# Performance work log

Hardware: AMD Instinct MI355X
Metric: run time of the kernel (lower is better)

The kernel has to match this reference:

```python
import jax, jax.numpy as jnp
import numpy as np

# Static configuration (mirrors the list of reconstruction_blocks)
B, F, D, H = 16384, 64, 32, 64
CARDS = ([4, 8, 16, 32] * 8) + [1] * 32  # 32 categorical + 32 numerical features
CMAX = max(CARDS)                         # pad all per-feature output dims to CMAX
TOTAL = sum(CARDS)                        # 512 = concat output width
# flat column indices selecting the valid (unpadded) outputs per feature
_flat = np.concatenate([np.arange(c) + f * CMAX for f, c in enumerate(CARDS)])
FLAT_IDX = jnp.asarray(_flat, dtype=jnp.int32)


def setup_inputs() -> dict:
    key = jax.random.key(0)
    k0, k1, k2 = jax.random.split(key, 3)
    return {
        "inputs": jax.random.normal(k0, (B, F, D), dtype=jnp.float32),
        # per-feature hidden layer: Dense(D -> H)
        "W1": jax.random.normal(k1, (F, D, H), dtype=jnp.float32) / np.float32(np.sqrt(D)),
        "b1": jnp.zeros((F, H), dtype=jnp.float32),
        # per-feature output layer, padded to CMAX columns (only CARDS[f] are used)
        "W2": jax.random.normal(k2, (F, H, CMAX), dtype=jnp.float32) / np.float32(np.sqrt(H)),
        "b2": jnp.zeros((F, CMAX), dtype=jnp.float32),
    }


def reference(inputs, W1, b1, W2, b2):
    # Batched grouped-GEMM over all per-feature MLP blocks at once.
    h = jax.nn.relu(jnp.einsum('bfd,fdh->bfh', inputs, W1) + b1)       # [B,F,H]
    out_pad = jnp.einsum('bfh,fhc->bfc', h, W2) + b2                   # [B,F,CMAX]
    # concat of per-feature outputs (varying widths) == gather of valid columns
    return out_pad.reshape(B, F * CMAX)[:, FLAT_IDX]                   # [B,TOTAL]
```

## Files before the change

### kernel.cpp

```cpp
#include <hip/hip_runtime.h>

typedef __attribute__((ext_vector_type(8))) short short8;
typedef __attribute__((ext_vector_type(4))) float f32x4;
typedef __attribute__((ext_vector_type(4))) unsigned short u16x4;

#define DI __device__ __forceinline__

namespace {
constexpr int TOT_ = 512;
constexpr int XROW = 2048;
constexpr int BT_  = 256;
constexpr int NB_  = (16384 / BT_) * 64;
}

DI unsigned short f2bf(float v) {
    __bf16 h = (__bf16)v;
    return __builtin_bit_cast(unsigned short, h);
}

__global__ __launch_bounds__(256)
void recon_kernel(const float* __restrict__ x, const float* __restrict__ W1,
                  const float* __restrict__ b1, const float* __restrict__ W2,
                  const float* __restrict__ b2, float* __restrict__ out)
{
    __shared__ __align__(16) unsigned short w1t[64 * 32];
    __shared__ __align__(16) unsigned short w2t[32 * 64];
    __shared__ __align__(16) unsigned short hb[4][16 * 64];

    const int bid   = blockIdx.x;
    const int f     = (bid >> 3) & 63;
    const int btile = ((bid & 7) << 3) | (bid >> 9);

    const int tid  = threadIdx.x;
    const int lane = tid & 63;
    const int wv   = tid >> 6;
    const int l15  = lane & 15;
    const int kg   = lane >> 4;
    const int swz  = (l15 & 7) << 3;

    {
        const int e0 = tid * 8;
        const float* W1f = W1 + f * 2048;
        const float* W2f = W2 + f * 2048;
        f32x4 v0 = *(const f32x4*)(W1f + e0);
        f32x4 v1 = *(const f32x4*)(W1f + e0 + 4);
        f32x4 u0 = *(const f32x4*)(W2f + e0);
        f32x4 u1 = *(const f32x4*)(W2f + e0 + 4);
#pragma unroll
        for (int j = 0; j < 8; ++j) {
            int e = e0 + j;
            float v = (j < 4) ? v0[j] : v1[j - 4];
            w1t[(e & 63) * 32 + (e >> 6)] = f2bf(v);
            float u = (j < 4) ? u0[j] : u1[j - 4];
            w2t[(e & 31) * 64 + (e >> 5)] = f2bf(u);
        }
    }
    __syncthreads();

    short8 w1b[4];
#pragma unroll
    for (int nt = 0; nt < 4; ++nt)
        w1b[nt] = *(const short8*)&w1t[(nt * 16 + l15) * 32 + kg * 8];

    short8 w2b[2][2];
#pragma unroll
    for (int nt = 0; nt < 2; ++nt)
#pragma unroll
        for (int ks = 0; ks < 2; ++ks)
            w2b[nt][ks] = *(const short8*)&w2t[(nt * 16 + l15) * 64 + ks * 32 + kg * 8];

    f32x4 b1q[4], b2q[2];
#pragma unroll
    for (int nt = 0; nt < 4; ++nt) b1q[nt] = *(const f32x4*)(b1 + f * 64 + nt * 16 + kg * 4);
#pragma unroll
    for (int nt = 0; nt < 2; ++nt) b2q[nt] = *(const f32x4*)(b2 + f * 32 + nt * 16 + kg * 4);

    int card, off;
    if (f < 32) { card = 4 << (f & 3); off = (f >> 2) * 60 + card - 4; }
    else        { card = 1;            off = 480 + (f - 32); }

    unsigned short* hw = hb[wv];
    const f32x4 zero = {0.f, 0.f, 0.f, 0.f};
    const int b0 = btile * BT_ + wv * 64;

    f32x4 xa[4][2];
#pragma unroll
    for (int t = 0; t < 4; ++t) {
        const float* xr = x + (size_t)(b0 + t * 16 + l15) * XROW + f * 32 + kg * 8;
        xa[t][0] = *(const f32x4*)xr;
        xa[t][1] = *(const f32x4*)(xr + 4);
    }

#pragma unroll
    for (int t = 0; t < 4; ++t) {
        short8 af;
#pragma unroll
        for (int j = 0; j < 4; ++j) {
            af[j]     = (short)f2bf(xa[t][0][j]);
            af[4 + j] = (short)f2bf(xa[t][1][j]);
        }

        f32x4 c1[4];
#pragma unroll
        for (int nt = 0; nt < 4; ++nt)
            c1[nt] = __builtin_amdgcn_mfma_f32_16x16x32_bf16(w1b[nt], af, zero, 0, 0, 0);

#pragma unroll
        for (int nt = 0; nt < 4; ++nt) {
            u16x4 hv;
#pragma unroll
            for (int j = 0; j < 4; ++j) {
                float v = c1[nt][j] + b1q[nt][j];
                hv[j] = f2bf(v > 0.f ? v : 0.f);
            }
            *(u16x4*)&hw[(l15 * 64 + nt * 16 + kg * 4) ^ swz] = hv;
        }

        short8 ha[2];
#pragma unroll
        for (int ks = 0; ks < 2; ++ks)
            ha[ks] = *(const short8*)&hw[(l15 * 64 + ks * 32 + kg * 8) ^ swz];

        f32x4 c2[2];
        c2[0] = __builtin_amdgcn_mfma_f32_16x16x32_bf16(w2b[0][0], ha[0], zero, 0, 0, 0);
        c2[0] = __builtin_amdgcn_mfma_f32_16x16x32_bf16(w2b[0][1], ha[1], c2[0], 0, 0, 0);
        if (card == 32) {
            c2[1] = __builtin_amdgcn_mfma_f32_16x16x32_bf16(w2b[1][0], ha[0], zero, 0, 0, 0);
            c2[1] = __builtin_amdgcn_mfma_f32_16x16x32_bf16(w2b[1][1], ha[1], c2[1], 0, 0, 0);
        }

        const int row = b0 + t * 16 + l15;
        if (card > 1) {
            const int ntiles = (card == 32) ? 2 : 1;
            for (int nt = 0; nt < ntiles; ++nt) {
                if (kg * 4 < card - nt * 16) {
                    f32x4 v;
#pragma unroll
                    for (int j = 0; j < 4; ++j) v[j] = c2[nt][j] + b2q[nt][j];
                    *(f32x4*)(out + (size_t)row * TOT_ + off + nt * 16 + kg * 4) = v;
                }
            }
        } else {
            if (kg == 0)
                out[(size_t)row * TOT_ + off] = c2[0][0] + b2q[0][0];
        }
    }
}

extern "C" void kernel_launch(void* const* d_in, const int* in_sizes, int n_in,
                              void* d_out, int out_size, void* d_ws, size_t ws_size,
                              hipStream_t stream) {
    const float* x  = (const float*)d_in[0];
    const float* W1 = (const float*)d_in[1];
    const float* b1 = (const float*)d_in[2];
    const float* W2 = (const float*)d_in[3];
    const float* b2 = (const float*)d_in[4];
    float* out = (float*)d_out;
    recon_kernel<<<NB_, 256, 0, stream>>>(x, W1, b1, W2, b2, out);
}
```

Before: 39.61 us.

## Use larger row tiles per block with 2 waves and software-prefetched x loads

Each block now covers 512 rows with two waves of 256 rows each, instead of 256 rows with four waves. This halves the grid size and amortizes the per-block weight conversion and transpose into LDS over more rows. Inside each wave the rows are handled in four 64-row chunks, and the next chunk's x loads are issued before the current chunk's MFMA work so memory latency overlaps compute. The costs are fewer resident waves per block and higher register pressure from the prefetch buffers, which could hurt latency hiding.

```diff
diff --git a/kernel.cpp b/kernel.cpp
--- a/kernel.cpp
+++ b/kernel.cpp
@@ -9,8 +9,8 @@
 namespace {
 constexpr int TOT_ = 512;
 constexpr int XROW = 2048;
-constexpr int BT_  = 256;
-constexpr int NB_  = (16384 / BT_) * 64;
+constexpr int RPB  = 512;
+constexpr int NB_  = (16384 / RPB) * 64;
 }
 
 DI unsigned short f2bf(float v) {
@@ -18,18 +18,20 @@
     return __builtin_bit_cast(unsigned short, h);
 }
 
-__global__ __launch_bounds__(256)
+__global__ __launch_bounds__(128, 3)
 void recon_kernel(const float* __restrict__ x, const float* __restrict__ W1,
                   const float* __restrict__ b1, const float* __restrict__ W2,
                   const float* __restrict__ b2, float* __restrict__ out)
 {
     __shared__ __align__(16) unsigned short w1t[64 * 32];
     __shared__ __align__(16) unsigned short w2t[32 * 64];
-    __shared__ __align__(16) unsigned short hb[4][16 * 64];
+    __shared__ __align__(16) unsigned short hb[2][16 * 64];
 
-    const int bid   = blockIdx.x;
-    const int f     = (bid >> 3) & 63;
-    const int btile = ((bid & 7) << 3) | (bid >> 9);
+    const int bid = blockIdx.x;
+    const int xcd = bid & 7;
+    const int ii  = bid >> 3;
+    const int f   = ii & 63;
+    const int rg  = (xcd << 2) | (ii >> 6);
 
     const int tid  = threadIdx.x;
     const int lane = tid & 63;
@@ -39,20 +41,20 @@
     const int swz  = (l15 & 7) << 3;
 
     {
-        const int e0 = tid * 8;
+        const int e0 = tid * 16;
         const float* W1f = W1 + f * 2048;
         const float* W2f = W2 + f * 2048;
-        f32x4 v0 = *(const f32x4*)(W1f + e0);
-        f32x4 v1 = *(const f32x4*)(W1f + e0 + 4);
-        f32x4 u0 = *(const f32x4*)(W2f + e0);
-        f32x4 u1 = *(const f32x4*)(W2f + e0 + 4);
+        f32x4 v[4], u[4];
 #pragma unroll
-        for (int j = 0; j < 8; ++j) {
+        for (int q = 0; q < 4; ++q) {
+            v[q] = *(const f32x4*)(W1f + e0 + q * 4);
+            u[q] = *(const f32x4*)(W2f + e0 + q * 4);
+        }
+#pragma unroll
+        for (int j = 0; j < 16; ++j) {
             int e = e0 + j;
-            float v = (j < 4) ? v0[j] : v1[j - 4];
-            w1t[(e & 63) * 32 + (e >> 6)] = f2bf(v);
-            float u = (j < 4) ? u0[j] : u1[j - 4];
-            w2t[(e & 31) * 64 + (e >> 5)] = f2bf(u);
+            w1t[(e & 63) * 32 + (e >> 6)] = f2bf(v[j >> 2][j & 3]);
+            w2t[(e & 31) * 64 + (e >> 5)] = f2bf(u[j >> 2][j & 3]);
         }
     }
     __syncthreads();
@@ -81,68 +83,77 @@
 
     unsigned short* hw = hb[wv];
     const f32x4 zero = {0.f, 0.f, 0.f, 0.f};
-    const int b0 = btile * BT_ + wv * 64;
+    const int r0 = rg * RPB + wv * 256;
+    const float* xb = x + (size_t)(r0 + l15) * XROW + f * 32 + kg * 8;
 
-    f32x4 xa[4][2];
+    f32x4 xv[4][2];
 #pragma unroll
     for (int t = 0; t < 4; ++t) {
-        const float* xr = x + (size_t)(b0 + t * 16 + l15) * XROW + f * 32 + kg * 8;
-        xa[t][0] = *(const f32x4*)xr;
-        xa[t][1] = *(const f32x4*)(xr + 4);
+        const float* p = xb + (size_t)(t * 16) * XROW;
+        xv[t][0] = *(const f32x4*)p;
+        xv[t][1] = *(const f32x4*)(p + 4);
     }
 
 #pragma unroll
-    for (int t = 0; t < 4; ++t) {
-        short8 af;
+    for (int rt = 0; rt < 4; ++rt) {
 #pragma unroll
-        for (int j = 0; j < 4; ++j) {
-            af[j]     = (short)f2bf(xa[t][0][j]);
-            af[4 + j] = (short)f2bf(xa[t][1][j]);
-        }
+        for (int t = 0; t < 4; ++t) {
+            short8 af;
+#pragma unroll
+            for (int j = 0; j < 4; ++j) {
+                af[j]     = (short)f2bf(xv[t][0][j]);
+                af[4 + j] = (short)f2bf(xv[t][1][j]);
+            }
+            if (rt < 3) {
+                const float* p = xb + (size_t)((rt + 1) * 64 + t * 16) * XROW;
+                xv[t][0] = *(const f32x4*)p;
+                xv[t][1] = *(const f32x4*)(p + 4);
+            }
 
-        f32x4 c1[4];
+            f32x4 c1[4];
 #pragma unroll
-        for (int nt = 0; nt < 4; ++nt)
-            c1[nt] = __builtin_amdgcn_mfma_f32_16x16x32_bf16(w1b[nt], af, zero, 0, 0, 0);
+            for (int nt = 0; nt < 4; ++nt)
+                c1[nt] = __builtin_amdgcn_mfma_f32_16x16x32_bf16(w1b[nt], af, zero, 0, 0, 0);
 
 #pragma unroll
-        for (int nt = 0; nt < 4; ++nt) {
-            u16x4 hv;
+            for (int nt = 0; nt < 4; ++nt) {
+                u16x4 hv;
 #pragma unroll
-            for (int j = 0; j < 4; ++j) {
-                float v = c1[nt][j] + b1q[nt][j];
-                hv[j] = f2bf(v > 0.f ? v : 0.f);
+                for (int j = 0; j < 4; ++j) {
+                    float v = c1[nt][j] + b1q[nt][j];
+                    hv[j] = f2bf(v > 0.f ? v : 0.f);
+                }
+                *(u16x4*)&hw[(l15 * 64 + nt * 16 + kg * 4) ^ swz] = hv;
             }
-            *(u16x4*)&hw[(l15 * 64 + nt * 16 + kg * 4) ^ swz] = hv;
-        }
 
-        short8 ha[2];
+            short8 ha[2];
 #pragma unroll
-        for (int ks = 0; ks < 2; ++ks)
-            ha[ks] = *(const short8*)&hw[(l15 * 64 + ks * 32 + kg * 8) ^ swz];
+            for (int ks = 0; ks < 2; ++ks)
+                ha[ks] = *(const short8*)&hw[(l15 * 64 + ks * 32 + kg * 8) ^ swz];
 
-        f32x4 c2[2];
-        c2[0] = __builtin_amdgcn_mfma_f32_16x16x32_bf16(w2b[0][0], ha[0], zero, 0, 0, 0);
-        c2[0] = __builtin_amdgcn_mfma_f32_16x16x32_bf16(w2b[0][1], ha[1], c2[0], 0, 0, 0);
-        if (card == 32) {
-            c2[1] = __builtin_amdgcn_mfma_f32_16x16x32_bf16(w2b[1][0], ha[0], zero, 0, 0, 0);
-            c2[1] = __builtin_amdgcn_mfma_f32_16x16x32_bf16(w2b[1][1], ha[1], c2[1], 0, 0, 0);
-        }
+            f32x4 c2[2];
+            c2[0] = __builtin_amdgcn_mfma_f32_16x16x32_bf16(w2b[0][0], ha[0], zero, 0, 0, 0);
+            c2[0] = __builtin_amdgcn_mfma_f32_16x16x32_bf16(w2b[0][1], ha[1], c2[0], 0, 0, 0);
+            if (card == 32) {
+                c2[1] = __builtin_amdgcn_mfma_f32_16x16x32_bf16(w2b[1][0], ha[0], zero, 0, 0, 0);
+                c2[1] = __builtin_amdgcn_mfma_f32_16x16x32_bf16(w2b[1][1], ha[1], c2[1], 0, 0, 0);
+            }
 
-        const int row = b0 + t * 16 + l15;
-        if (card > 1) {
-            const int ntiles = (card == 32) ? 2 : 1;
-            for (int nt = 0; nt < ntiles; ++nt) {
-                if (kg * 4 < card - nt * 16) {
-                    f32x4 v;
+            const int row = r0 + rt * 64 + t * 16 + l15;
+            if (card > 1) {
+                const int ntiles = (card == 32) ? 2 : 1;
+                for (int nt = 0; nt < ntiles; ++nt) {
+                    if (kg * 4 < card - nt * 16) {
+                        f32x4 v;
 #pragma unroll
-                    for (int j = 0; j < 4; ++j) v[j] = c2[nt][j] + b2q[nt][j];
-                    *(f32x4*)(out + (size_t)row * TOT_ + off + nt * 16 + kg * 4) = v;
+                        for (int j = 0; j < 4; ++j) v[j] = c2[nt][j] + b2q[nt][j];
+                        *(f32x4*)(out + (size_t)row * TOT_ + off + nt * 16 + kg * 4) = v;
+                    }
                 }
+            } else {
+                if (kg == 0)
+                    out[(size_t)row * TOT_ + off] = c2[0][0] + b2q[0][0];
             }
-        } else {
-            if (kg == 0)
-                out[(size_t)row * TOT_ + off] = c2[0][0] + b2q[0][0];
         }
     }
 }
@@ -156,5 +167,5 @@
     const float* W2 = (const float*)d_in[3];
     const float* b2 = (const float*)d_in[4];
     float* out = (float*)d_out;
-    recon_kernel<<<NB_, 256, 0, stream>>>(x, W1, b1, W2, b2, out);
+    recon_kernel<<<NB_, 128, 0, stream>>>(x, W1, b1, W2, b2, out);
 }
```

After: 43.56 us. 10.0% more time.

## Hoist x loads, skip full W2 staging for scalar features, fold biases into MFMA

Applied to the files above, without the earlier changes.

Issues the per-block x loads before weight staging so their global latency overlaps the W1/W2 conversion and barrier. Numerical features (card=1) no longer load and transpose the full padded W2 tile into shared memory; they gather only column 0 straight from global. Biases are passed as the MFMA accumulator input instead of being added afterwards, and launch bounds request 4 blocks per CU. This trades the x load registers being live across the barrier, which adds register pressure, for lower weight-load traffic and more latency hiding.

```diff
diff --git a/kernel.cpp b/kernel.cpp
--- a/kernel.cpp
+++ b/kernel.cpp
@@ -18,7 +18,7 @@
     return __builtin_bit_cast(unsigned short, h);
 }
 
-__global__ __launch_bounds__(256)
+__global__ __launch_bounds__(256, 4)
 void recon_kernel(const float* __restrict__ x, const float* __restrict__ W1,
                   const float* __restrict__ b1, const float* __restrict__ W2,
                   const float* __restrict__ b2, float* __restrict__ out)
@@ -37,22 +37,39 @@
     const int l15  = lane & 15;
     const int kg   = lane >> 4;
     const int swz  = (l15 & 7) << 3;
+    const bool catf = (f < 32);
 
+    const int b0 = btile * BT_ + wv * 64;
+
+    f32x4 xa[4][2];
+#pragma unroll
+    for (int t = 0; t < 4; ++t) {
+        const float* xr = x + (size_t)(b0 + t * 16 + l15) * XROW + f * 32 + kg * 8;
+        xa[t][0] = *(const f32x4*)xr;
+        xa[t][1] = *(const f32x4*)(xr + 4);
+    }
+
+    const float* W1f = W1 + f * 2048;
+    const float* W2f = W2 + f * 2048;
     {
         const int e0 = tid * 8;
-        const float* W1f = W1 + f * 2048;
-        const float* W2f = W2 + f * 2048;
         f32x4 v0 = *(const f32x4*)(W1f + e0);
         f32x4 v1 = *(const f32x4*)(W1f + e0 + 4);
-        f32x4 u0 = *(const f32x4*)(W2f + e0);
-        f32x4 u1 = *(const f32x4*)(W2f + e0 + 4);
+        if (catf) {
+            f32x4 u0 = *(const f32x4*)(W2f + e0);
+            f32x4 u1 = *(const f32x4*)(W2f + e0 + 4);
+#pragma unroll
+            for (int j = 0; j < 8; ++j) {
+                int e = e0 + j;
+                float u = (j < 4) ? u0[j] : u1[j - 4];
+                w2t[(e & 31) * 64 + (e >> 5)] = f2bf(u);
+            }
+        }
 #pragma unroll
         for (int j = 0; j < 8; ++j) {
             int e = e0 + j;
             float v = (j < 4) ? v0[j] : v1[j - 4];
             w1t[(e & 63) * 32 + (e >> 6)] = f2bf(v);
-            float u = (j < 4) ? u0[j] : u1[j - 4];
-            w2t[(e & 31) * 64 + (e >> 5)] = f2bf(u);
         }
     }
     __syncthreads();
@@ -62,12 +79,20 @@
     for (int nt = 0; nt < 4; ++nt)
         w1b[nt] = *(const short8*)&w1t[(nt * 16 + l15) * 32 + kg * 8];
 
-    short8 w2b[2][2];
+    short8 w2b[2][2] = {};
+    if (catf) {
 #pragma unroll
-    for (int nt = 0; nt < 2; ++nt)
+        for (int nt = 0; nt < 2; ++nt)
+#pragma unroll
+            for (int ks = 0; ks < 2; ++ks)
+                w2b[nt][ks] = *(const short8*)&w2t[(nt * 16 + l15) * 64 + ks * 32 + kg * 8];
+    } else {
 #pragma unroll
         for (int ks = 0; ks < 2; ++ks)
-            w2b[nt][ks] = *(const short8*)&w2t[(nt * 16 + l15) * 64 + ks * 32 + kg * 8];
+#pragma unroll
+            for (int j = 0; j < 8; ++j)
+                w2b[0][ks][j] = (short)f2bf(W2f[(ks * 32 + kg * 8 + j) * 32]);
+    }
 
     f32x4 b1q[4], b2q[2];
 #pragma unroll
@@ -76,20 +101,10 @@
     for (int nt = 0; nt < 2; ++nt) b2q[nt] = *(const f32x4*)(b2 + f * 32 + nt * 16 + kg * 4);
 
     int card, off;
-    if (f < 32) { card = 4 << (f & 3); off = (f >> 2) * 60 + card - 4; }
-    else        { card = 1;            off = 480 + (f - 32); }
+    if (catf) { card = 4 << (f & 3); off = (f >> 2) * 60 + card - 4; }
+    else      { card = 1;            off = 480 + (f - 32); }
 
     unsigned short* hw = hb[wv];
-    const f32x4 zero = {0.f, 0.f, 0.f, 0.f};
-    const int b0 = btile * BT_ + wv * 64;
-
-    f32x4 xa[4][2];
-#pragma unroll
-    for (int t = 0; t < 4; ++t) {
-        const float* xr = x + (size_t)(b0 + t * 16 + l15) * XROW + f * 32 + kg * 8;
-        xa[t][0] = *(const f32x4*)xr;
-        xa[t][1] = *(const f32x4*)(xr + 4);
-    }
 
 #pragma unroll
     for (int t = 0; t < 4; ++t) {
@@ -103,14 +118,14 @@
         f32x4 c1[4];
 #pragma unroll
         for (int nt = 0; nt < 4; ++nt)
-            c1[nt] = __builtin_amdgcn_mfma_f32_16x16x32_bf16(w1b[nt], af, zero, 0, 0, 0);
+            c1[nt] = __builtin_amdgcn_mfma_f32_16x16x32_bf16(w1b[nt], af, b1q[nt], 0, 0, 0);
 
 #pragma unroll
         for (int nt = 0; nt < 4; ++nt) {
             u16x4 hv;
 #pragma unroll
             for (int j = 0; j < 4; ++j) {
-                float v = c1[nt][j] + b1q[nt][j];
+                float v = c1[nt][j];
                 hv[j] = f2bf(v > 0.f ? v : 0.f);
             }
             *(u16x4*)&hw[(l15 * 64 + nt * 16 + kg * 4) ^ swz] = hv;
@@ -122,10 +137,10 @@
             ha[ks] = *(const short8*)&hw[(l15 * 64 + ks * 32 + kg * 8) ^ swz];
 
         f32x4 c2[2];
-        c2[0] = __builtin_amdgcn_mfma_f32_16x16x32_bf16(w2b[0][0], ha[0], zero, 0, 0, 0);
+        c2[0] = __builtin_amdgcn_mfma_f32_16x16x32_bf16(w2b[0][0], ha[0], b2q[0], 0, 0, 0);
         c2[0] = __builtin_amdgcn_mfma_f32_16x16x32_bf16(w2b[0][1], ha[1], c2[0], 0, 0, 0);
         if (card == 32) {
-            c2[1] = __builtin_amdgcn_mfma_f32_16x16x32_bf16(w2b[1][0], ha[0], zero, 0, 0, 0);
+            c2[1] = __builtin_amdgcn_mfma_f32_16x16x32_bf16(w2b[1][0], ha[0], b2q[1], 0, 0, 0);
             c2[1] = __builtin_amdgcn_mfma_f32_16x16x32_bf16(w2b[1][1], ha[1], c2[1], 0, 0, 0);
         }
 
@@ -136,13 +151,13 @@
                 if (kg * 4 < card - nt * 16) {
                     f32x4 v;
 #pragma unroll
-                    for (int j = 0; j < 4; ++j) v[j] = c2[nt][j] + b2q[nt][j];
+                    for (int j = 0; j < 4; ++j) v[j] = c2[nt][j];
                     *(f32x4*)(out + (size_t)row * TOT_ + off + nt * 16 + kg * 4) = v;
                 }
             }
         } else {
             if (kg == 0)
-                out[(size_t)row * TOT_ + off] = c2[0][0] + b2q[0][0];
+                out[(size_t)row * TOT_ + off] = c2[0][0];
         }
     }
 }
```

Result: no change. 40.19 us (+1.5%).

## Pre-convert weights in a prep kernel and tile by batch rows across all features

Applied to the files above, without the earlier changes.

A small prep kernel converts and transposes W1/W2 to bf16 once per call and stores them in the workspace. The main kernel now assigns one block per 32 batch rows, stages those rows' full input (all 64 features) into LDS as bf16 in two passes, and loops over features inside the block, reading weights from global/L2. This makes input reads and output writes fully contiguous per row and drops the per-block weight conversion, at the cost of an extra launch, weight reloads from cache per feature, and a large LDS footprint that limits occupancy. Biases are folded into the MFMA accumulator initialisation.

```diff
diff --git a/kernel.cpp b/kernel.cpp
--- a/kernel.cpp
+++ b/kernel.cpp
@@ -3,14 +3,15 @@
 typedef __attribute__((ext_vector_type(8))) short short8;
 typedef __attribute__((ext_vector_type(4))) float f32x4;
 typedef __attribute__((ext_vector_type(4))) unsigned short u16x4;
+typedef __attribute__((ext_vector_type(8))) unsigned short u16x8;
 
 #define DI __device__ __forceinline__
 
 namespace {
 constexpr int TOT_ = 512;
 constexpr int XROW = 2048;
-constexpr int BT_  = 256;
-constexpr int NB_  = (16384 / BT_) * 64;
+constexpr int RPB  = 32;
+constexpr int NBM  = 16384 / RPB;
 }
 
 DI unsigned short f2bf(float v) {
@@ -19,130 +20,128 @@
 }
 
 __global__ __launch_bounds__(256)
-void recon_kernel(const float* __restrict__ x, const float* __restrict__ W1,
-                  const float* __restrict__ b1, const float* __restrict__ W2,
-                  const float* __restrict__ b2, float* __restrict__ out)
+void prep_kernel(const float* __restrict__ W1, const float* __restrict__ W2,
+                 unsigned short* __restrict__ ws)
 {
-    __shared__ __align__(16) unsigned short w1t[64 * 32];
-    __shared__ __align__(16) unsigned short w2t[32 * 64];
-    __shared__ __align__(16) unsigned short hb[4][16 * 64];
-
-    const int bid   = blockIdx.x;
-    const int f     = (bid >> 3) & 63;
-    const int btile = ((bid & 7) << 3) | (bid >> 9);
-
-    const int tid  = threadIdx.x;
-    const int lane = tid & 63;
-    const int wv   = tid >> 6;
-    const int l15  = lane & 15;
-    const int kg   = lane >> 4;
-    const int swz  = (l15 & 7) << 3;
-
-    {
-        const int e0 = tid * 8;
-        const float* W1f = W1 + f * 2048;
-        const float* W2f = W2 + f * 2048;
-        f32x4 v0 = *(const f32x4*)(W1f + e0);
-        f32x4 v1 = *(const f32x4*)(W1f + e0 + 4);
-        f32x4 u0 = *(const f32x4*)(W2f + e0);
-        f32x4 u1 = *(const f32x4*)(W2f + e0 + 4);
+    __shared__ __align__(16) unsigned short w1t[2048];
+    __shared__ __align__(16) unsigned short w2t[2048];
+    const int f = blockIdx.x, tid = threadIdx.x, e0 = tid * 8;
+    const float* W1f = W1 + f * 2048;
+    const float* W2f = W2 + f * 2048;
+    f32x4 v0 = *(const f32x4*)(W1f + e0), v1 = *(const f32x4*)(W1f + e0 + 4);
+    f32x4 u0 = *(const f32x4*)(W2f + e0), u1 = *(const f32x4*)(W2f + e0 + 4);
 #pragma unroll
-        for (int j = 0; j < 8; ++j) {
-            int e = e0 + j;
-            float v = (j < 4) ? v0[j] : v1[j - 4];
-            w1t[(e & 63) * 32 + (e >> 6)] = f2bf(v);
-            float u = (j < 4) ? u0[j] : u1[j - 4];
-            w2t[(e & 31) * 64 + (e >> 5)] = f2bf(u);
-        }
+    for (int j = 0; j < 8; ++j) {
+        int e = e0 + j;
+        w1t[(e & 63) * 32 + (e >> 6)] = f2bf(j < 4 ? v0[j] : v1[j - 4]);
+        w2t[(e & 31) * 64 + (e >> 5)] = f2bf(j < 4 ? u0[j] : u1[j - 4]);
     }
     __syncthreads();
+    *(short8*)(ws + f * 2048 + e0)          = *(const short8*)(w1t + e0);
+    *(short8*)(ws + 131072 + f * 2048 + e0) = *(const short8*)(w2t + e0);
+}
 
-    short8 w1b[4];
+__global__ __launch_bounds__(512)
+void recon_kernel(const float* __restrict__ x, const unsigned short* __restrict__ ws,
+                  const float* __restrict__ b1, const float* __restrict__ b2,
+                  float* __restrict__ out)
+{
+    __shared__ __align__(16) unsigned short slab[32 * 1024];
+    __shared__ __align__(16) unsigned short hb[8][1024];
+
+    const int r0   = blockIdx.x * RPB;
+    const int tid  = threadIdx.x, lane = tid & 63, wv = tid >> 6;
+    const int mt   = wv >> 2;
+    const int fg   = wv & 3;
+    const int l15  = lane & 15, kg = lane >> 4;
+    const int swz  = (l15 & 7) << 3;
+    const unsigned short* ws1 = ws;
+    const unsigned short* ws2 = ws + 131072;
+    unsigned short* hw = hb[wv];
+
+    const int srow = wv >> 1;
+    const int su   = (wv & 1) * 64 + lane;
+
+    for (int p = 0; p < 2; ++p) {
+        if (p) __syncthreads();
 #pragma unroll
-    for (int nt = 0; nt < 4; ++nt)
-        w1b[nt] = *(const short8*)&w1t[(nt * 16 + l15) * 32 + kg * 8];
+        for (int it = 0; it < 8; ++it) {
+            const int row = it * 4 + srow;
+            const float* xp = x + (size_t)(r0 + row) * XROW + p * 1024 + su * 8;
+            f32x4 a = *(const f32x4*)xp, b = *(const f32x4*)(xp + 4);
+            u16x8 hv;
+#pragma unroll
+            for (int j = 0; j < 4; ++j) { hv[j] = f2bf(a[j]); hv[4 + j] = f2bf(b[j]); }
+            *(u16x8*)&slab[(row * 1024 + su * 8) ^ ((row & 7) << 3)] = hv;
+        }
+        __syncthreads();
 
-    short8 w2b[2][2];
+#pragma unroll 2
+        for (int i = 0; i < 8; ++i) {
+            const int f = p * 32 + fg * 8 + i;
+            short8 af = *(const short8*)
+                &slab[((mt * 16 + l15) * 1024 + (fg * 8 + i) * 32 + kg * 8) ^ swz];
+
+            const unsigned short* w1f = ws1 + f * 2048;
+            f32x4 c1[4];
 #pragma unroll
-    for (int nt = 0; nt < 2; ++nt)
+            for (int nt = 0; nt < 4; ++nt) {
+                short8 w1b = *(const short8*)&w1f[(nt * 16 + l15) * 32 + kg * 8];
+                f32x4 b1q  = *(const f32x4*)(b1 + f * 64 + nt * 16 + kg * 4);
+                c1[nt] = __builtin_amdgcn_mfma_f32_16x16x32_bf16(w1b, af, b1q, 0, 0, 0);
+            }
 #pragma unroll
-        for (int ks = 0; ks < 2; ++ks)
-            w2b[nt][ks] = *(const short8*)&w2t[(nt * 16 + l15) * 64 + ks * 32 + kg * 8];
+            for (int nt = 0; nt < 4; ++nt) {
+                u16x4 hv;
+#pragma unroll
+                for (int j = 0; j < 4; ++j) {
+                    float v = c1[nt][j];
+                    hv[j] = f2bf(v > 0.f ? v : 0.f);
+                }
+                *(u16x4*)&hw[(l15 * 64 + nt * 16 + kg * 4) ^ swz] = hv;
+            }
+            short8 ha0 = *(const short8*)&hw[(l15 * 64 + kg * 8) ^ swz];
+            short8 ha1 = *(const short8*)&hw[(l15 * 64 + 32 + kg * 8) ^ swz];
 
-    f32x4 b1q[4], b2q[2];
+            const unsigned short* w2f = ws2 + f * 2048;
+            const int row = r0 + mt * 16 + l15;
+            if (p == 0) {
+                const int card = 4 << (i & 3);
+                const int off  = (f >> 2) * 60 + card - 4;
+                f32x4 c2[2];
+                {
+                    short8 w200 = *(const short8*)&w2f[l15 * 64 + kg * 8];
+                    short8 w201 = *(const short8*)&w2f[l15 * 64 + 32 + kg * 8];
+                    f32x4 b2q0  = *(const f32x4*)(b2 + f * 32 + kg * 4);
+                    c2[0] = __builtin_amdgcn_mfma_f32_16x16x32_bf16(w200, ha0, b2q0, 0, 0, 0);
+                    c2[0] = __builtin_amdgcn_mfma_f32_16x16x32_bf16(w201, ha1, c2[0], 0, 0, 0);
+                }
+                if (card == 32) {
+                    short8 w210 = *(const short8*)&w2f[(16 + l15) * 64 + kg * 8];
+                    short8 w211 = *(const short8*)&w2f[(16 + l15) * 64 + 32 + kg * 8];
+                    f32x4 b2q1  = *(const f32x4*)(b2 + f * 32 + 16 + kg * 4);
+                    c2[1] = __builtin_amdgcn_mfma_f32_16x16x32_bf16(w210, ha0, b2q1, 0, 0, 0);
+                    c2[1] = __builtin_amdgcn_mfma_f32_16x16x32_bf16(w211, ha1, c2[1], 0, 0, 0);
+                }
+                const int ntiles = (card == 32) ? 2 : 1;
+                for (int nt = 0; nt < ntiles; ++nt) {
+                    if (kg * 4 < card - nt * 16) {
+                        f32x4 v;
 #pragma unroll
-    for (int nt = 0; nt < 4; ++nt) b1q[nt] = *(const f32x4*)(b1 + f * 64 + nt * 16 + kg * 4);
-#pragma unroll
-    for (int nt = 0; nt < 2; ++nt) b2q[nt] = *(const f32x4*)(b2 + f * 32 + nt * 16 + kg * 4);
-
-    int card, off;
-    if (f < 32) { card = 4 << (f & 3); off = (f >> 2) * 60 + card - 4; }
-    else        { card = 1;            off = 480 + (f - 32); }
-
-    unsigned short* hw = hb[wv];
-    const f32x4 zero = {0.f, 0.f, 0.f, 0.f};
-    const int b0 = btile * BT_ + wv * 64;
-
-    f32x4 xa[4][2];
-#pragma unroll
-    for (int t = 0; t < 4; ++t) {
-        const float* xr = x + (size_t)(b0 + t * 16 + l15) * XROW + f * 32 + kg * 8;
-        xa[t][0] = *(const f32x4*)xr;
-        xa[t][1] = *(const f32x4*)(xr + 4);
-    }
-
-#pragma unroll
-    for (int t = 0; t < 4; ++t) {
-        short8 af;
-#pragma unroll
-        for (int j = 0; j < 4; ++j) {
-            af[j]     = (short)f2bf(xa[t][0][j]);
-            af[4 + j] = (short)f2bf(xa[t][1][j]);
-        }
-
-        f32x4 c1[4];
-#pragma unroll
-        for (int nt = 0; nt < 4; ++nt)
-            c1[nt] = __builtin_amdgcn_mfma_f32_16x16x32_bf16(w1b[nt], af, zero, 0, 0, 0);
-
-#pragma unroll
-        for (int nt = 0; nt < 4; ++nt) {
-            u16x4 hv;
-#pragma unroll
-            for (int j = 0; j < 4; ++j) {
-                float v = c1[nt][j] + b1q[nt][j];
-                hv[j] = f2bf(v > 0.f ? v : 0.f);
+                        for (int j = 0; j < 4; ++j) v[j] = c2[nt][j];
+                        *(f32x4*)(out + (size_t)row * TOT_ + off + nt * 16 + kg * 4) = v;
+                    }
+                }
+            } else {
+                short8 w20 = *(const short8*)&w2f[kg * 8];
+                short8 w21 = *(const short8*)&w2f[32 + kg * 8];
+                f32x4 b2q0 = *(const f32x4*)(b2 + f * 32 + kg * 4);
+                f32x4 c2;
+                c2 = __builtin_amdgcn_mfma_f32_16x16x32_bf16(w20, ha0, b2q0, 0, 0, 0);
+                c2 = __builtin_amdgcn_mfma_f32_16x16x32_bf16(w21, ha1, c2, 0, 0, 0);
+                if (kg == 0)
+                    out[(size_t)row * TOT_ + 480 + (f - 32)] = c2[0];
             }
-            *(u16x4*)&hw[(l15 * 64 + nt * 16 + kg * 4) ^ swz] = hv;
-        }
-
-        short8 ha[2];
-#pragma unroll
-        for (int ks = 0; ks < 2; ++ks)
-            ha[ks] = *(const short8*)&hw[(l15 * 64 + ks * 32 + kg * 8) ^ swz];
-
-        f32x4 c2[2];
-        c2[0] = __builtin_amdgcn_mfma_f32_16x16x32_bf16(w2b[0][0], ha[0], zero, 0, 0, 0);
-        c2[0] = __builtin_amdgcn_mfma_f32_16x16x32_bf16(w2b[0][1], ha[1], c2[0], 0, 0, 0);
-        if (card == 32) {
-            c2[1] = __builtin_amdgcn_mfma_f32_16x16x32_bf16(w2b[1][0], ha[0], zero, 0, 0, 0);
-            c2[1] = __builtin_amdgcn_mfma_f32_16x16x32_bf16(w2b[1][1], ha[1], c2[1], 0, 0, 0);
-        }
-
-        const int row = b0 + t * 16 + l15;
-        if (card > 1) {
-            const int ntiles = (card == 32) ? 2 : 1;
-            for (int nt = 0; nt < ntiles; ++nt) {
-                if (kg * 4 < card - nt * 16) {
-                    f32x4 v;
-#pragma unroll
-                    for (int j = 0; j < 4; ++j) v[j] = c2[nt][j] + b2q[nt][j];
-                    *(f32x4*)(out + (size_t)row * TOT_ + off + nt * 16 + kg * 4) = v;
-                }
-            }
-        } else {
-            if (kg == 0)
-                out[(size_t)row * TOT_ + off] = c2[0][0] + b2q[0][0];
         }
     }
 }
@@ -156,5 +155,7 @@
     const float* W2 = (const float*)d_in[3];
     const float* b2 = (const float*)d_in[4];
     float* out = (float*)d_out;
-    recon_kernel<<<NB_, 256, 0, stream>>>(x, W1, b1, W2, b2, out);
+    unsigned short* ws = (unsigned short*)d_ws;
+    prep_kernel<<<64, 256, 0, stream>>>(W1, W2, ws);
+    recon_kernel<<<NBM, 512, 0, stream>>>(x, ws, b1, b2, out);
 }
```

Result: slower. 79.69 us (+101.2%).
